# Kernel optimization log

Measured on AMD Instinct MI355X. Metric: run time of the kernel, lower is better.

Reference implementation:

```python
import jax, jax.numpy as jnp
import numpy as np


def _pair_indices(n_beads):
    # Replicates the torch loop ordering: all pairs at offset 1, then offset 2, ...
    i_list, j_list = [], []
    for off in range(1, n_beads):
        i = np.arange(n_beads - off)
        i_list.append(i)
        j_list.append(i + off)
    return np.concatenate(i_list), np.concatenate(j_list)


def setup_inputs() -> dict:
    key = jax.random.key(0)
    data = jax.random.normal(key, (4096, 128, 3), dtype=jnp.float32)
    return {"data": data}


def _features(data):
    n = data.shape[1]
    i_idx, j_idx = _pair_indices(n)  # static numpy index arrays

    # All pairwise distances, ordered by bead offset (matches torch loop order)
    dvec = data[:, j_idx, :] - data[:, i_idx, :]          # [B, P, 3]
    distances = jnp.linalg.norm(dvec, axis=2)             # [B, P]

    # Adjacent bond vectors: x[j+1] - x[j]
    adj = data[:, 1:, :] - data[:, :-1, :]                # [B, n-1, 3]

    # Planar angles over consecutive bond-vector pairs
    a0, a1 = adj[:, : n - 2, :], adj[:, 1 : n - 1, :]
    angles = jnp.arccos(
        jnp.sum(a0 * a1, axis=2)
        / jnp.linalg.norm(a0, axis=2)
        / jnp.linalg.norm(a1, axis=2)
    )                                                     # [B, n-2]

    # Dihedrals
    cpa = jnp.cross(a0, a1, axis=2)                       # [B, n-2, 3]
    plane = jnp.cross(cpa[:, 1 : n - 2, :], adj[:, 1 : n - 2, :], axis=2)  # [B, n-3, 3]
    c0, c1 = cpa[:, : n - 3, :], cpa[:, 1 : n - 2, :]
    nc0 = jnp.linalg.norm(c0, axis=2)
    dihedral_cos = jnp.sum(c0 * c1, axis=2) / nc0 / jnp.linalg.norm(c1, axis=2)
    p0 = plane[:, : n - 3, :]
    dihedral_sin = jnp.sum(c0 * p0, axis=2) / nc0 / jnp.linalg.norm(p0, axis=2)

    return jnp.concatenate([distances, angles, dihedral_cos, dihedral_sin], axis=1)


def reference(data):
    return _features(data)
```

## Files before the change

kernel.cpp:

```cpp
#include <hip/hip_runtime.h>
#include <math.h>

constexpr int NB    = 128;
constexpr int NPAIR = NB * (NB - 1) / 2;
constexpr int NANG  = NB - 2;
constexpr int NDIH  = NB - 3;
constexpr int ROW   = NPAIR + NANG + 2 * NDIH;

__global__ __launch_bounds__(1024, 8) void protein_feat_kernel(
        const float* __restrict__ data, float* __restrict__ out) {
    __shared__ float4 s4[NB];
    const int b  = blockIdx.x;
    const int t  = threadIdx.x;
    const int tb = t & 127;
    const int g  = t >> 7;
    const float* src = data + (size_t)b * (NB * 3);

    if (t < NB)
        s4[t] = make_float4(src[3 * t], src[3 * t + 1], src[3 * t + 2], 0.0f);
    __syncthreads();

    float* orow = out + (size_t)b * ROW;

    float px[4], py[4], pz[4];
    #pragma unroll
    for (int k = 0; k < 4; ++k) {
        int idx = tb - k; if (idx < 0) idx = 0;
        float4 v = s4[idx];
        px[k] = v.x; py[k] = v.y; pz[k] = v.z;
    }

    #pragma unroll
    for (int m = 0; m < 4; ++m) {
        const int off = 16 * g + 4 * m + 1;
        const int len = NB - off;
        const int bk0 = (off - 1) * (2 * NB - off) / 2;
        const int bk1 = bk0 + len;
        const int bk2 = bk1 + len - 1;
        const int bk3 = bk2 + len - 2;
        if (tb < len) {
            float4 pj = s4[tb + off];
            float dx, dy, dz, d;
            dx = pj.x - px[0]; dy = pj.y - py[0]; dz = pj.z - pz[0];
            d = __builtin_amdgcn_sqrtf(dx*dx + dy*dy + dz*dz);
            orow[bk0 + tb] = d;
            dx = pj.x - px[1]; dy = pj.y - py[1]; dz = pj.z - pz[1];
            d = __builtin_amdgcn_sqrtf(dx*dx + dy*dy + dz*dz);
            if (tb >= 1) orow[bk1 + tb - 1] = d;
            dx = pj.x - px[2]; dy = pj.y - py[2]; dz = pj.z - pz[2];
            d = __builtin_amdgcn_sqrtf(dx*dx + dy*dy + dz*dz);
            if (tb >= 2) orow[bk2 + tb - 2] = d;
            dx = pj.x - px[3]; dy = pj.y - py[3]; dz = pj.z - pz[3];
            d = __builtin_amdgcn_sqrtf(dx*dx + dy*dy + dz*dz);
            if (tb >= 3) orow[bk3 + tb - 3] = d;
        }
    }

    const int v = t;
    if (v < NANG + 2 * NDIH) {
        if (v < NANG) {
            int a = v;
            float4 p0 = s4[a], p1 = s4[a + 1], p2 = s4[a + 2];
            float a0x = p1.x - p0.x, a0y = p1.y - p0.y, a0z = p1.z - p0.z;
            float a1x = p2.x - p1.x, a1y = p2.y - p1.y, a1z = p2.z - p1.z;
            float d  = a0x * a1x + a0y * a1y + a0z * a1z;
            float r0 = rsqrtf(a0x * a0x + a0y * a0y + a0z * a0z);
            float r1 = rsqrtf(a1x * a1x + a1y * a1y + a1z * a1z);
            float c  = d * r0 * r1;
            c = fminf(1.0f, fmaxf(-1.0f, c));
            orow[NPAIR + a] = acosf(c);
        } else {
            int a = (v < NANG + NDIH) ? (v - NANG) : (v - NANG - NDIH);
            float4 p0 = s4[a], p1 = s4[a + 1], p2 = s4[a + 2], p3 = s4[a + 3];
            float e0x = p1.x - p0.x, e0y = p1.y - p0.y, e0z = p1.z - p0.z;
            float e1x = p2.x - p1.x, e1y = p2.y - p1.y, e1z = p2.z - p1.z;
            float e2x = p3.x - p2.x, e2y = p3.y - p2.y, e2z = p3.z - p2.z;
            float c0x = e0y * e1z - e0z * e1y;
            float c0y = e0z * e1x - e0x * e1z;
            float c0z = e0x * e1y - e0y * e1x;
            float c1x = e1y * e2z - e1z * e2y;
            float c1y = e1z * e2x - e1x * e2z;
            float c1z = e1x * e2y - e1y * e2x;
            float rn0 = rsqrtf(c0x * c0x + c0y * c0y + c0z * c0z);
            if (v < NANG + NDIH) {
                float d   = c0x * c1x + c0y * c1y + c0z * c1z;
                float rn1 = rsqrtf(c1x * c1x + c1y * c1y + c1z * c1z);
                orow[NPAIR + NANG + a] = d * rn0 * rn1;
            } else {
                float qx = c1y * e1z - c1z * e1y;
                float qy = c1z * e1x - c1x * e1z;
                float qz = c1x * e1y - c1y * e1x;
                float d  = c0x * qx + c0y * qy + c0z * qz;
                float rp = rsqrtf(qx * qx + qy * qy + qz * qz);
                orow[NPAIR + NANG + NDIH + a] = d * rn0 * rp;
            }
        }
    }
}

extern "C" void kernel_launch(void* const* d_in, const int* in_sizes, int n_in,
                              void* d_out, int out_size, void* d_ws, size_t ws_size,
                              hipStream_t stream) {
    const float* data = (const float*)d_in[0];
    float* out = (float*)d_out;
    const int batch = in_sizes[0] / (NB * 3);
    protein_feat_kernel<<<batch, 1024, 0, stream>>>(data, out);
}
```

Before: 30.78 us.

## Stage pair distances in shared memory and write out with float4 stores

Pair distances are now written to a shared-memory row buffer instead of directly to global memory. Each 64-lane wave then copies its contiguous slice of eight bead offsets to the output with aligned float4 stores. Work is remapped from 128-thread groups to waves, each lane handling a low and a high bead index. The aim is fewer, wider, aligned global stores in place of scalar stores at misaligned positions. The cost is about 32 KB of extra LDS per block, which may cut the number of resident blocks, plus an extra LDS round trip.

```diff
diff --git a/kernel.cpp b/kernel.cpp
--- a/kernel.cpp
+++ b/kernel.cpp
@@ -10,10 +10,11 @@
 __global__ __launch_bounds__(1024, 8) void protein_feat_kernel(
         const float* __restrict__ data, float* __restrict__ out) {
     __shared__ float4 s4[NB];
-    const int b  = blockIdx.x;
-    const int t  = threadIdx.x;
-    const int tb = t & 127;
-    const int g  = t >> 7;
+    __shared__ float  sfeat[NPAIR];
+    const int b = blockIdx.x;
+    const int t = threadIdx.x;
+    const int l = t & 63;
+    const int w = t >> 6;
     const float* src = data + (size_t)b * (NB * 3);
 
     if (t < NB)
@@ -22,38 +23,69 @@
 
     float* orow = out + (size_t)b * ROW;
 
-    float px[4], py[4], pz[4];
+    float pxL[4], pyL[4], pzL[4], pxH[4], pyH[4], pzH[4];
     #pragma unroll
     for (int k = 0; k < 4; ++k) {
-        int idx = tb - k; if (idx < 0) idx = 0;
-        float4 v = s4[idx];
-        px[k] = v.x; py[k] = v.y; pz[k] = v.z;
+        int iL = l - k; if (iL < 0) iL = 0;
+        float4 v = s4[iL];
+        pxL[k] = v.x; pyL[k] = v.y; pzL[k] = v.z;
+        float4 u = s4[l + 64 - k];
+        pxH[k] = u.x; pyH[k] = u.y; pzH[k] = u.z;
     }
 
+    const int off_base = 8 * w + 1;
+
     #pragma unroll
-    for (int m = 0; m < 4; ++m) {
-        const int off = 16 * g + 4 * m + 1;
-        const int len = NB - off;
-        const int bk0 = (off - 1) * (2 * NB - off) / 2;
-        const int bk1 = bk0 + len;
-        const int bk2 = bk1 + len - 1;
-        const int bk3 = bk2 + len - 2;
-        if (tb < len) {
-            float4 pj = s4[tb + off];
+    for (int m = 0; m < 2; ++m) {
+        const int off0 = off_base + 4 * m;
+        const int len0 = NB - off0;
+        const int bk0  = (off0 - 1) * (2 * NB - off0) / 2;
+        const int bk1  = bk0 + len0;
+        const int bk2  = bk1 + len0 - 1;
+        const int bk3  = bk2 + len0 - 2;
+
+        if (l < len0) {
+            float4 pj = s4[l + off0];
             float dx, dy, dz, d;
-            dx = pj.x - px[0]; dy = pj.y - py[0]; dz = pj.z - pz[0];
+            dx = pj.x - pxL[0]; dy = pj.y - pyL[0]; dz = pj.z - pzL[0];
             d = __builtin_amdgcn_sqrtf(dx*dx + dy*dy + dz*dz);
-            orow[bk0 + tb] = d;
-            dx = pj.x - px[1]; dy = pj.y - py[1]; dz = pj.z - pz[1];
+            sfeat[bk0 + l] = d;
+            dx = pj.x - pxL[1]; dy = pj.y - pyL[1]; dz = pj.z - pzL[1];
             d = __builtin_amdgcn_sqrtf(dx*dx + dy*dy + dz*dz);
-            if (tb >= 1) orow[bk1 + tb - 1] = d;
-            dx = pj.x - px[2]; dy = pj.y - py[2]; dz = pj.z - pz[2];
+            if (l >= 1) sfeat[bk1 + l - 1] = d;
+            dx = pj.x - pxL[2]; dy = pj.y - pyL[2]; dz = pj.z - pzL[2];
             d = __builtin_amdgcn_sqrtf(dx*dx + dy*dy + dz*dz);
-            if (tb >= 2) orow[bk2 + tb - 2] = d;
-            dx = pj.x - px[3]; dy = pj.y - py[3]; dz = pj.z - pz[3];
+            if (l >= 2) sfeat[bk2 + l - 2] = d;
+            dx = pj.x - pxL[3]; dy = pj.y - pyL[3]; dz = pj.z - pzL[3];
             d = __builtin_amdgcn_sqrtf(dx*dx + dy*dy + dz*dz);
-            if (tb >= 3) orow[bk3 + tb - 3] = d;
+            if (l >= 3) sfeat[bk3 + l - 3] = d;
         }
+        const int P = l + 64;
+        if (P < len0) {
+            float4 pj = s4[P + off0];
+            float dx, dy, dz, d;
+            dx = pj.x - pxH[0]; dy = pj.y - pyH[0]; dz = pj.z - pzH[0];
+            d = __builtin_amdgcn_sqrtf(dx*dx + dy*dy + dz*dz);
+            sfeat[bk0 + P] = d;
+            dx = pj.x - pxH[1]; dy = pj.y - pyH[1]; dz = pj.z - pzH[1];
+            d = __builtin_amdgcn_sqrtf(dx*dx + dy*dy + dz*dz);
+            sfeat[bk1 + P - 1] = d;
+            dx = pj.x - pxH[2]; dy = pj.y - pyH[2]; dz = pj.z - pzH[2];
+            d = __builtin_amdgcn_sqrtf(dx*dx + dy*dy + dz*dz);
+            sfeat[bk2 + P - 2] = d;
+            dx = pj.x - pxH[3]; dy = pj.y - pyH[3]; dz = pj.z - pzH[3];
+            d = __builtin_amdgcn_sqrtf(dx*dx + dy*dy + dz*dz);
+            sfeat[bk3 + P - 3] = d;
+        }
+    }
+
+    {
+        const int base4 = ((off_base - 1) * (2 * NB - off_base) / 2) >> 2;
+        const int nf4   = (988 - 64 * w) >> 2;
+        const float4* sf4 = (const float4*)sfeat;
+        float4* dst = (float4*)orow;
+        for (int f = l; f < nf4; f += 64)
+            dst[base4 + f] = sf4[base4 + f];
     }
 
     const int v = t;
```

After: 33.06 us. 7.4% more time.
